# Kernel tuning notes

Measured on AMD Instinct MI355X. Metric: run time of the kernel, lower is better.

## Reference

```python
import jax, jax.numpy as jnp
import numpy as np

H = 512       # hidden_size
T_OUT = 168   # output_len


def _cell(x, h, c, Wih, Whh, b):
    # PyTorch LSTM cell, gate order (i, f, g, o); b = b_ih + b_hh merged.
    g = x @ Wih.T + h @ Whh.T + b
    i, f, gg, o = jnp.split(g, 4, axis=-1)
    c = jax.nn.sigmoid(f) * c + jax.nn.sigmoid(i) * jnp.tanh(gg)
    h = jax.nn.sigmoid(o) * jnp.tanh(c)
    return h, c


def setup_inputs() -> dict:
    key = jax.random.key(0)
    ks = jax.random.split(key, 20)
    B, T_IN, F = 1024, 336, 16
    s = 1.0 / np.sqrt(H)

    def w(k, shape):
        return (jax.random.normal(k, shape, dtype=jnp.float32) * s).astype(jnp.float32)

    return {
        "x": jax.random.normal(ks[0], (B, T_IN, F), dtype=jnp.float32),
        "enc_Wih0": w(ks[1], (4 * H, F)),
        "enc_Whh0": w(ks[2], (4 * H, H)),
        "enc_b0": w(ks[3], (4 * H,)),
        "enc_Wih1": w(ks[4], (4 * H, H)),
        "enc_Whh1": w(ks[5], (4 * H, H)),
        "enc_b1": w(ks[6], (4 * H,)),
        "dec_Wih0": w(ks[7], (4 * H, 1)),
        "dec_Whh0": w(ks[8], (4 * H, H)),
        "dec_b0": w(ks[9], (4 * H,)),
        "dec_Wih1": w(ks[10], (4 * H, H)),
        "dec_Whh1": w(ks[11], (4 * H, H)),
        "dec_b1": w(ks[12], (4 * H,)),
        "fc_W1": w(ks[13], (H // 2, H)),
        "fc_b1": w(ks[14], (H // 2,)),
        "fc_W2": w(ks[15], (1, H // 2)),
        "fc_b2": w(ks[16], (1,)),
    }


def reference(x, enc_Wih0, enc_Whh0, enc_b0, enc_Wih1, enc_Whh1, enc_b1,
              dec_Wih0, dec_Whh0, dec_b0, dec_Wih1, dec_Whh1, dec_b1,
              fc_W1, fc_b1, fc_W2, fc_b2):
    # Inference mode: no teacher forcing, dropout disabled (identity).
    B = x.shape[0]
    xs = jnp.swapaxes(x, 0, 1)  # [T_in, B, F]
    z = jnp.zeros((B, H), x.dtype)

    def enc_layer(seq, Wih, Whh, b):
        def step(carry, xt):
            h, c = carry
            h, c = _cell(xt, h, c, Wih, Whh, b)
            return (h, c), h
        (h, c), ys = jax.lax.scan(step, (z, z), seq)
        return ys, h, c

    ys0, h0, c0 = enc_layer(xs, enc_Wih0, enc_Whh0, enc_b0)
    _, h1, c1 = enc_layer(ys0, enc_Wih1, enc_Whh1, enc_b1)

    y0 = jnp.zeros((B, 1), x.dtype)  # decoder_input = zeros(batch,1,1) squeezed

    def dec_step(carry, _):
        h0, c0, h1, c1, y = carry
        h0, c0 = _cell(y, h0, c0, dec_Wih0, dec_Whh0, dec_b0)
        h1, c1 = _cell(h0, h1, c1, dec_Wih1, dec_Whh1, dec_b1)
        hid = jnp.maximum(h1 @ fc_W1.T + fc_b1, 0.0)
        pred = jnp.maximum(hid @ fc_W2.T + fc_b2, 0.0)  # [B, 1]
        return (h0, c0, h1, c1, pred), pred[:, 0]

    _, outs = jax.lax.scan(dec_step, (h0, c0, h1, c1, y0), None, length=T_OUT)
    return jnp.swapaxes(outs, 0, 1)  # [B, T_OUT]
```

## Files before the change

kernel.cpp:

```cpp
#include <hip/hip_runtime.h>
#include <math.h>

#define TPB 512
#define NBLK 256

typedef unsigned short u16;
typedef unsigned char u8;
typedef float f32x4 __attribute__((ext_vector_type(4)));
typedef short s16x8 __attribute__((ext_vector_type(8)));
typedef unsigned int u32x4 __attribute__((ext_vector_type(4)));
typedef unsigned int u32x2 __attribute__((ext_vector_type(2)));

__device__ __forceinline__ u16 f2bf(float f) {
  unsigned u = __float_as_uint(f);
  unsigned r = (u + 0x7FFFu + ((u >> 16) & 1u)) >> 16;
  return (u16)r;
}
__device__ __forceinline__ float bf2f(u16 b) { return __uint_as_float(((unsigned)b) << 16); }
__device__ __forceinline__ float sigm(float x) { return 1.f / (1.f + expf(-x)); }

__device__ __forceinline__ f32x4 mfma_bf16(s16x8 a, s16x8 b, f32x4 c) {
  return __builtin_amdgcn_mfma_f32_16x16x32_bf16(a, b, c, 0, 0, 0);
}

__device__ __forceinline__ unsigned pk2(unsigned wd, int j) {
  int b0 = ((int)(wd << ((3 - j) * 8))) >> 24;
  int b1 = ((int)(wd << ((2 - j) * 8))) >> 24;
  float f0 = (float)b0 * 0.0078125f;
  float f1 = (float)b1 * 0.0078125f;
  return (__float_as_uint(f0) >> 16) | (__float_as_uint(f1) & 0xFFFF0000u);
}
__device__ __forceinline__ s16x8 unpk8(u32x2 wv) {
  s16x8 o;
#pragma unroll
  for (int j = 0; j < 4; ++j) {
    int b0 = ((int)(wv[0] << ((3 - j) * 8))) >> 24;
    float f0 = (float)b0 * 0.0078125f;
    o[j] = (short)(__float_as_uint(f0) >> 16);
    int b1 = ((int)(wv[1] << ((3 - j) * 8))) >> 24;
    float f1 = (float)b1 * 0.0078125f;
    o[4 + j] = (short)(__float_as_uint(f1) >> 16);
  }
  return o;
}

__device__ __forceinline__ u32x4 ld_sc1_x4(const void* p) {
  u32x4 d;
  asm volatile("global_load_dwordx4 %0, %1, off sc1"
               : "=v"(d) : "v"((unsigned long long)p) : "memory");
  return d;
}
__device__ __forceinline__ u32x2 ld_sc1_x2(const void* p) {
  u32x2 d;
  asm volatile("global_load_dwordx2 %0, %1, off sc1"
               : "=v"(d) : "v"((unsigned long long)p) : "memory");
  return d;
}
__device__ __forceinline__ s16x8 ld_b16x8(const void* p) {
  s16x8 d;
  asm volatile("global_load_dwordx4 %0, %1, off"
               : "=v"(d) : "v"((unsigned long long)p) : "memory");
  return d;
}
__device__ __forceinline__ void st_sc1_x4(void* p, u32x4 v) {
  asm volatile("global_store_dwordx4 %0, %1, off sc1"
               :: "v"((unsigned long long)p), "v"(v) : "memory");
}
__device__ __forceinline__ void wait_vm0() { asm volatile("s_waitcnt vmcnt(0)" ::: "memory"); }
#define WAITVM(n) asm volatile("s_waitcnt vmcnt(" #n ")" ::: "memory")
__device__ __forceinline__ void pin(u32x4& v) { asm volatile("" : "+v"(v)); }
__device__ __forceinline__ void pin(u32x2& v) { asm volatile("" : "+v"(v)); }
__device__ __forceinline__ void pin(s16x8& v) { asm volatile("" : "+v"(v)); }

struct KParams {
  const float* x;
  float* out;
  unsigned long long* cx;
  unsigned long long* cg;
  u8* h0h[2]; u8* h1h[2];
  const u16 *we0h, *we0l;
  const u16 *we1h, *we1l;
  const u16 *wd0h, *wd0l;
  const u16 *wd1h, *wd1l;
  const u16 *wfh;
  const float *be0, *be1, *bd0, *bd1, *wyp;
  const float *fcb1, *fcw2, *fcb2;
};

__global__ void zero_ws(uint4* p, long n) {
  uint4 z = {0u, 0u, 0u, 0u};
  for (long i = (long)blockIdx.x * blockDim.x + threadIdx.x; i < n; i += (long)gridDim.x * blockDim.x)
    p[i] = z;
}

__global__ void prep_w(const float* __restrict__ Wih, const float* __restrict__ Whh,
                       const float* __restrict__ bias,
                       u16* __restrict__ dhi, u16* __restrict__ dlo,
                       float* __restrict__ bias_p, float* __restrict__ wy_p,
                       int mode, int nchunks) {
  long total = (long)nchunks * 2048 * 32;
  for (long i = (long)blockIdx.x * blockDim.x + threadIdx.x; i < total; i += (long)gridDim.x * blockDim.x) {
    int kk = (int)(i & 31);
    long r1 = i >> 5;
    int n = (int)(r1 & 2047);
    int c = (int)(r1 >> 11);
    int h = n >> 2, g = n & 3;
    int no = g * 512 + h;
    float wv;
    if (mode == 0)      wv = (c < 16) ? Whh[no * 512 + c * 32 + kk] : (kk < 16 ? Wih[no * 16 + kk] : 0.f);
    else if (mode == 1) wv = (c < 16) ? Wih[no * 512 + c * 32 + kk] : Whh[no * 512 + (c - 16) * 32 + kk];
    else                wv = Whh[no * 512 + c * 32 + kk];
    u16 hb = f2bf(wv);
    dhi[i] = hb;
    dlo[i] = f2bf(wv - bf2f(hb));
    if (i < 2048) {
      int nn = (int)i, hh = nn >> 2, gg = nn & 3, noo = gg * 512 + hh;
      bias_p[nn] = bias[noo];
      if (mode == 2) wy_p[nn] = Wih[noo];
    }
  }
}

__global__ void prep_fc(const float* __restrict__ W1, u16* __restrict__ dhi) {
  int total = 16 * 256 * 32;
  for (int i = blockIdx.x * blockDim.x + threadIdx.x; i < total; i += gridDim.x * blockDim.x) {
    int kk = i & 31, n = (i >> 5) & 255, c = i >> 13;
    dhi[i] = f2bf(W1[n * 512 + c * 32 + kk]);
  }
}

__device__ __forceinline__ void gbar(const KParams& P, int mgrp, unsigned long long bi) {
  wait_vm0();
  __syncthreads();
  if (threadIdx.x == 0) {
    unsigned long long* ctr = &P.cx[mgrp * 32];
    __hip_atomic_fetch_add(ctr, 1ULL, __ATOMIC_RELAXED, __HIP_MEMORY_SCOPE_AGENT);
    unsigned long long t0 = __builtin_amdgcn_s_memrealtime();
    while (__hip_atomic_load(ctr, __ATOMIC_RELAXED, __HIP_MEMORY_SCOPE_AGENT) < bi * 16ULL) {
      __builtin_amdgcn_s_sleep(2);
      if (__builtin_amdgcn_s_memrealtime() - t0 > 300000000ULL) {
        P.out[0] = 1e9f;
        break;
      }
    }
  }
  __syncthreads();
}

template <int NCT, bool TWOA, bool HASX, bool HASY>
__device__ __forceinline__ void lstm_phase(
    const KParams& P, int m_tile, int n_tile,
    const u8* A1h, const u8* A2h,
    const u16* WBh, const u16* WBl,
    const float* __restrict__ bias_p, const float* __restrict__ wyp, int t,
    float (&creg)[4], u8* Hh, char* smem, const float* yb) {
  constexpr int NST = NCT / 2;
  const int tid = threadIdx.x;
  const int w = tid >> 6, lane = tid & 63, r = lane & 15, q = lane >> 4;
  const int m0 = m_tile * 64, n0 = n_tile * 128;
  u16* sA = (u16*)smem;
  const int rr = (tid >> 2) & 63, seg = tid & 3, chA = tid >> 8;

  f32x4 acc[4];
#pragma unroll
  for (int mr = 0; mr < 4; ++mr) acc[mr] = (f32x4){0.f, 0.f, 0.f, 0.f};

  u32x2 ab[6];
  s16x8 bb[2][4];
  const int a_elem = (m0 + rr) * 32 + seg * 8;
  const int b_elem = (n0 + w * 16 + r) * 32 + q * 8;

  auto issueA = [&](int s) {
    int c = s * 2 + chA;
    const u8* base = A1h;
    if (TWOA && c >= 16) { base = A2h; c -= 16; }
    ab[s % 6] = ld_sc1_x2(base + c * 32768 + a_elem);
  };
  auto issueB = [&](int s) {
#pragma unroll
    for (int i = 0; i < 4; ++i) {
      int ch = i >> 1, hl = i & 1;
      int c = s * 2 + ch;
      bb[s & 1][i] = ld_b16x8((hl ? WBl : WBh) + c * 65536 + b_elem);
    }
  };

  issueA(0); issueB(0); issueA(1); issueB(1);
  issueA(2); issueA(3); issueA(4); issueA(5);

#pragma unroll
  for (int s = 0; s < NST; ++s) {
    if (s == NST - 1)       WAITVM(0);
    else if (s <= 1)        WAITVM(9);
    else if (s <= NST - 6)  WAITVM(6);
    else if (s == NST - 5)  WAITVM(5);
    else                    WAITVM(4);
    pin(ab[s % 6]);
#pragma unroll
    for (int i = 0; i < 4; ++i) pin(bb[s & 1][i]);
    u16* sAb = sA + (s & 1) * 5120;
    {
      u32x2 av = ab[s % 6];
      u32x4 w0;
      w0[0] = pk2(av[0], 0); w0[1] = pk2(av[0], 2);
      w0[2] = pk2(av[1], 0); w0[3] = pk2(av[1], 2);
      *(u32x4*)(sAb + (chA * 64 + rr) * 40 + seg * 8) = w0;
    }
    __syncthreads();
#pragma unroll
    for (int ch = 0; ch < 2; ++ch)
#pragma unroll
      for (int mr = 0; mr < 4; ++mr) {
        const s16x8 ah = *(const s16x8*)(sAb + (ch * 64 + mr * 16 + r) * 40 + q * 8);
        acc[mr] = mfma_bf16(ah, bb[s & 1][ch * 2 + 0], acc[mr]);
        acc[mr] = mfma_bf16(ah, bb[s & 1][ch * 2 + 1], acc[mr]);
      }
    if (s + 2 < NST) issueB(s + 2);
    if (s + 6 < NST) issueA(s + 6);
  }

  if (HASX) {
#pragma unroll
    for (int mr = 0; mr < 4; ++mr) {
      s16x8 axh;
#pragma unroll
      for (int j = 0; j < 8; ++j) axh[j] = 0;
      if (q < 2) {
        const float* xp = P.x + (((long)(m0 + mr * 16 + r) * 336 + t) * 16 + q * 8);
        float4 v0 = *(const float4*)xp;
        float4 v1 = *(const float4*)(xp + 4);
        float vv[8] = {v0.x, v0.y, v0.z, v0.w, v1.x, v1.y, v1.z, v1.w};
#pragma unroll
        for (int j = 0; j < 8; ++j) axh[j] = (short)f2bf(vv[j]);
      }
      long bo = ((long)16 * 2048 + n0 + w * 16 + r) * 32 + q * 8;
      acc[mr] = mfma_bf16(axh, *(const s16x8*)(WBh + bo), acc[mr]);
      acc[mr] = mfma_bf16(axh, *(const s16x8*)(WBl + bo), acc[mr]);
    }
  }

  __syncthreads();
  float* gbuf = (float*)smem;
#pragma unroll
  for (int mr = 0; mr < 4; ++mr)
#pragma unroll
    for (int reg = 0; reg < 4; ++reg)
      gbuf[(mr * 16 + q * 4 + reg) * 132 + (w * 16 + r)] = acc[mr][reg];
  __syncthreads();
  u8 hbv[4];
#pragma unroll
  for (int kk2 = 0; kk2 < 4; ++kk2) {
    int p = tid + kk2 * 512;
    int ml = p >> 5, hl2 = p & 31;
    f32x4 g4 = *(const f32x4*)(gbuf + ml * 132 + hl2 * 4);
    int nb = n0 + hl2 * 4;
    float g0 = g4[0] + bias_p[nb + 0];
    float g1 = g4[1] + bias_p[nb + 1];
    float g2 = g4[2] + bias_p[nb + 2];
    float g3 = g4[3] + bias_p[nb + 3];
    if (HASY) {
      float yv = yb[ml];
      g0 += yv * wyp[nb + 0];
      g1 += yv * wyp[nb + 1];
      g2 += yv * wyp[nb + 2];
      g3 += yv * wyp[nb + 3];
    }
    float ig = sigm(g0), fg = sigm(g1), gg = tanhf(g2), og = sigm(g3);
    float cn = fg * creg[kk2] + ig * gg;
    creg[kk2] = cn;
    int qi = __float2int_rn(og * tanhf(cn) * 128.f);
    qi = qi > 127 ? 127 : (qi < -127 ? -127 : qi);
    hbv[kk2] = (u8)qi;
  }
  __syncthreads();
  u8* lh = (u8*)smem;
#pragma unroll
  for (int kk2 = 0; kk2 < 4; ++kk2) {
    int p = tid + kk2 * 512;
    lh[(p >> 5) * 48 + (p & 31)] = hbv[kk2];
  }
  __syncthreads();
  if (tid < 128) {
    int rw = tid >> 1, sg = tid & 1;
    st_sc1_x4(Hh + (n_tile * 1024 + m0 + rw) * 32 + sg * 16,
              *(const u32x4*)(lh + rw * 48 + sg * 16));
  }
}

__device__ __forceinline__ void fc_inline(const KParams& P, int m_tile, int n_tile,
                                          const u8* Ah, int tOut, char* smem) {
  const int tid = threadIdx.x;
  const int w = tid >> 6, lane = tid & 63, r = lane & 15, q = lane >> 4;
  const int m0 = m_tile * 64;
  u8* sF = (u8*)smem;
  f32x4 af[4][2];
#pragma unroll
  for (int mr = 0; mr < 4; ++mr)
#pragma unroll
    for (int mi = 0; mi < 2; ++mi) af[mr][mi] = (f32x4){0.f, 0.f, 0.f, 0.f};

  u32x4 v1[2], v2[2];
#pragma unroll
  for (int j = 0; j < 2; ++j) {
    int idx = tid + j * 512;
    int c = idx >> 7, rw = (idx >> 1) & 63, sg = idx & 1;
    v1[j] = ld_sc1_x4(Ah + c * 32768 + (m0 + rw) * 32 + sg * 16);
  }
#pragma unroll
  for (int j = 0; j < 2; ++j) {
    int idx = tid + j * 512;
    int c = (idx >> 7) + 8, rw = (idx >> 1) & 63, sg = idx & 1;
    v2[j] = ld_sc1_x4(Ah + c * 32768 + (m0 + rw) * 32 + sg * 16);
  }
  WAITVM(2);
#pragma unroll
  for (int j = 0; j < 2; ++j) pin(v1[j]);
#pragma unroll
  for (int j = 0; j < 2; ++j) {
    int idx = tid + j * 512;
    int c = idx >> 7, rw = (idx >> 1) & 63, sg = idx & 1;
    *(u32x4*)(sF + (c * 64 + rw) * 48 + sg * 16) = v1[j];
  }
  __syncthreads();
#pragma unroll
  for (int pass = 0; pass < 2; ++pass) {
    for (int c = 0; c < 8; ++c)
#pragma unroll
      for (int mr = 0; mr < 4; ++mr) {
        const s16x8 ah = unpk8(*(const u32x2*)(sF + (c * 64 + mr * 16 + r) * 48 + q * 8));
#pragma unroll
        for (int mi = 0; mi < 2; ++mi) {
          int col = w * 32 + mi * 16 + r;
          af[mr][mi] = mfma_bf16(
              ah, *(const s16x8*)(P.wfh + ((pass * 8 + c) * 256 + col) * 32 + q * 8),
              af[mr][mi]);
        }
      }
    if (pass == 0) {
      wait_vm0();
#pragma unroll
      for (int j = 0; j < 2; ++j) pin(v2[j]);
      __syncthreads();
#pragma unroll
      for (int j = 0; j < 2; ++j) {
        int idx = tid + j * 512;
        int c = idx >> 7, rw = (idx >> 1) & 63, sg = idx & 1;
        *(u32x4*)(sF + (c * 64 + rw) * 48 + sg * 16) = v2[j];
      }
      __syncthreads();
    }
  }
  __syncthreads();
  u16* hidb = (u16*)smem;
#pragma unroll
  for (int mr = 0; mr < 4; ++mr)
#pragma unroll
    for (int mi = 0; mi < 2; ++mi)
#pragma unroll
      for (int reg = 0; reg < 4; ++reg) {
        int row = mr * 16 + q * 4 + reg, col = w * 32 + mi * 16 + r;
        hidb[row * 264 + col] = f2bf(fmaxf(af[mr][mi][reg] + P.fcb1[col], 0.f));
      }
  __syncthreads();
  float* part = (float*)(smem + 33792);
  if (tid < 256) {
    int m = tid >> 2, sg = tid & 3;
    float s = 0.f;
#pragma unroll
    for (int j = 0; j < 64; ++j)
      s += bf2f(hidb[m * 264 + sg * 64 + j]) * P.fcw2[sg * 64 + j];
    part[m * 5 + sg] = s;
  }
  __syncthreads();
  float* yb = (float*)(smem + 40960);
  if (tid < 64) {
    float s = P.fcb2[0] + part[tid * 5 + 0] + part[tid * 5 + 1] +
              part[tid * 5 + 2] + part[tid * 5 + 3];
    float pred = fmaxf(s, 0.f);
    yb[tid] = pred;
    if (n_tile == 0) P.out[(long)(m0 + tid) * 168 + tOut] = pred;
  }
  __syncthreads();
}

__global__ void __launch_bounds__(TPB, 2) lstm_seq(KParams P) {
  __shared__ __align__(16) char smem[41216];
  const int b = blockIdx.x;
  const int grp = b & 7;
  const int idx = b >> 3;
  const int n_tile = grp * 2 + (idx & 1);
  const int m_tile = idx >> 1;
  const float* yb = (const float*)(smem + 40960);
  unsigned long long bi = 0;
  int p0 = 0, p1 = 0;
  float c0r[4], c1r[4];
#pragma unroll
  for (int i = 0; i < 4; ++i) { c0r[i] = 0.f; c1r[i] = 0.f; }

  for (int p = 0; p <= 336; ++p) {
    if (p < 336)
      lstm_phase<16, false, true, false>(P, m_tile, n_tile, P.h0h[p0], nullptr,
                                         P.we0h, P.we0l, P.be0, nullptr, p, c0r,
                                         P.h0h[p0 ^ 1], smem, nullptr);
    if (p >= 1)
      lstm_phase<32, true, false, false>(P, m_tile, n_tile, P.h0h[p0], P.h1h[p1],
                                         P.we1h, P.we1l, P.be1, nullptr, 0, c1r,
                                         P.h1h[p1 ^ 1], smem, nullptr);
    if (p < 336) p0 ^= 1;
    if (p >= 1) p1 ^= 1;
    ++bi; gbar(P, m_tile, bi);
  }
  for (int t = 0; t < 168; ++t) {
    if (t > 0) {
      fc_inline(P, m_tile, n_tile, P.h1h[p1], t - 1, smem);
    } else {
      if (threadIdx.x < 64) ((float*)(smem + 40960))[threadIdx.x] = 0.f;
      __syncthreads();
    }
    lstm_phase<16, false, false, true>(P, m_tile, n_tile, P.h0h[p0], nullptr,
                                       P.wd0h, P.wd0l, P.bd0, P.wyp, 0, c0r,
                                       P.h0h[p0 ^ 1], smem, yb);
    p0 ^= 1; ++bi; gbar(P, m_tile, bi);
    lstm_phase<32, true, false, false>(P, m_tile, n_tile, P.h0h[p0], P.h1h[p1],
                                       P.wd1h, P.wd1l, P.bd1, nullptr, 0, c1r,
                                       P.h1h[p1 ^ 1], smem, nullptr);
    p1 ^= 1; ++bi; gbar(P, m_tile, bi);
  }
  fc_inline(P, m_tile, n_tile, P.h1h[p1], 167, smem);
}

extern "C" void kernel_launch(void* const* d_in, const int* in_sizes, int n_in,
                              void* d_out, int out_size, void* d_ws, size_t ws_size,
                              hipStream_t stream) {
  const float* x     = (const float*)d_in[0];
  const float* eWih0 = (const float*)d_in[1];
  const float* eWhh0 = (const float*)d_in[2];
  const float* eb0   = (const float*)d_in[3];
  const float* eWih1 = (const float*)d_in[4];
  const float* eWhh1 = (const float*)d_in[5];
  const float* eb1   = (const float*)d_in[6];
  const float* dWih0 = (const float*)d_in[7];
  const float* dWhh0 = (const float*)d_in[8];
  const float* db0   = (const float*)d_in[9];
  const float* dWih1 = (const float*)d_in[10];
  const float* dWhh1 = (const float*)d_in[11];
  const float* db1   = (const float*)d_in[12];
  const float* fcW1  = (const float*)d_in[13];
  const float* fcb1  = (const float*)d_in[14];
  const float* fcW2  = (const float*)d_in[15];
  const float* fcb2  = (const float*)d_in[16];

  char* ws = (char*)d_ws;
  unsigned long long* cx = (unsigned long long*)(ws + 0);
  unsigned long long* cg = (unsigned long long*)(ws + 4096);
  char* hb = ws + 8192;
  u8* h0h0 = (u8*)(hb + 0L * 1048576);
  u8* h0h1 = (u8*)(hb + 1L * 1048576);
  u8* h1h0 = (u8*)(hb + 2L * 1048576);
  u8* h1h1 = (u8*)(hb + 3L * 1048576);
  char* wb = hb + 4L * 1048576;
  u16* we0h = (u16*)wb; wb += 2228224L;
  u16* we0l = (u16*)wb; wb += 2228224L;
  u16* we1h = (u16*)wb; wb += 4194304L;
  u16* we1l = (u16*)wb; wb += 4194304L;
  u16* wd0h = (u16*)wb; wb += 2097152L;
  u16* wd0l = (u16*)wb; wb += 2097152L;
  u16* wd1h = (u16*)wb; wb += 4194304L;
  u16* wd1l = (u16*)wb; wb += 4194304L;
  u16* wfh  = (u16*)wb; wb += 262144L;
  float* be0 = (float*)wb; wb += 8192L;
  float* be1 = (float*)wb; wb += 8192L;
  float* bd0 = (float*)wb; wb += 8192L;
  float* bd1 = (float*)wb; wb += 8192L;
  float* wyp = (float*)wb; wb += 8192L;

  long zbytes = 8192L + 4L * 1048576L;
  zero_ws<<<1024, 256, 0, stream>>>((uint4*)ws, zbytes / 16);
  prep_w<<<2048, 256, 0, stream>>>(eWih0, eWhh0, eb0, we0h, we0l, be0, nullptr, 0, 17);
  prep_w<<<2048, 256, 0, stream>>>(eWih1, eWhh1, eb1, we1h, we1l, be1, nullptr, 1, 32);
  prep_w<<<2048, 256, 0, stream>>>(dWih0, dWhh0, db0, wd0h, wd0l, bd0, wyp, 2, 16);
  prep_w<<<2048, 256, 0, stream>>>(dWih1, dWhh1, db1, wd1h, wd1l, bd1, nullptr, 1, 32);
  prep_fc<<<512, 256, 0, stream>>>(fcW1, wfh);

  KParams P;
  P.x = x; P.out = (float*)d_out; P.cx = cx; P.cg = cg;
  P.h0h[0] = h0h0; P.h0h[1] = h0h1;
  P.h1h[0] = h1h0; P.h1h[1] = h1h1;
  P.we0h = we0h; P.we0l = we0l; P.we1h = we1h; P.we1l = we1l;
  P.wd0h = wd0h; P.wd0l = wd0l; P.wd1h = wd1h; P.wd1l = wd1l;
  P.wfh = wfh;
  P.be0 = be0; P.be1 = be1; P.bd0 = bd0; P.bd1 = bd1; P.wyp = wyp;
  P.fcb1 = fcb1; P.fcw2 = fcW2; P.fcb2 = fcb2;

  lstm_seq<<<NBLK, TPB, 0, stream>>>(P);
}
```

Measured before the change: 20.05 ms.

## Double threads per block to 1024 and split per-wave MFMA work across M

Raises the block size from 512 to 1024 threads. The 16 waves are arranged as a 2x8 grid over the 64x128 gate tile, so each wave handles 2 M-row tiles instead of 4. The FC stage likewise gives each wave one 16-column slice, and A loads shrink to one dword per thread. The aim is more latency hiding and shorter per-wave serial MFMA chains in this latency-bound persistent recurrent kernel. In exchange it adds register pressure under launch_bounds(1024,4), each B tile is now loaded by two waves, and __syncthreads barriers span more waves.

```diff
diff --git a/kernel.cpp b/kernel.cpp
--- a/kernel.cpp
+++ b/kernel.cpp
@@ -1,7 +1,7 @@
 #include <hip/hip_runtime.h>
 #include <math.h>
 
-#define TPB 512
+#define TPB 1024
 #define NBLK 256
 
 typedef unsigned short u16;
@@ -50,9 +50,9 @@
                : "=v"(d) : "v"((unsigned long long)p) : "memory");
   return d;
 }
-__device__ __forceinline__ u32x2 ld_sc1_x2(const void* p) {
-  u32x2 d;
-  asm volatile("global_load_dwordx2 %0, %1, off sc1"
+__device__ __forceinline__ unsigned ld_sc1_x1(const void* p) {
+  unsigned d;
+  asm volatile("global_load_dword %0, %1, off sc1"
                : "=v"(d) : "v"((unsigned long long)p) : "memory");
   return d;
 }
@@ -69,7 +69,7 @@
 __device__ __forceinline__ void wait_vm0() { asm volatile("s_waitcnt vmcnt(0)" ::: "memory"); }
 #define WAITVM(n) asm volatile("s_waitcnt vmcnt(" #n ")" ::: "memory")
 __device__ __forceinline__ void pin(u32x4& v) { asm volatile("" : "+v"(v)); }
-__device__ __forceinline__ void pin(u32x2& v) { asm volatile("" : "+v"(v)); }
+__device__ __forceinline__ void pin(unsigned& v) { asm volatile("" : "+v"(v)); }
 __device__ __forceinline__ void pin(s16x8& v) { asm volatile("" : "+v"(v)); }
 
 struct KParams {
@@ -153,28 +153,29 @@
     const u8* A1h, const u8* A2h,
     const u16* WBh, const u16* WBl,
     const float* __restrict__ bias_p, const float* __restrict__ wyp, int t,
-    float (&creg)[4], u8* Hh, char* smem, const float* yb) {
+    float (&creg)[2], u8* Hh, char* smem, const float* yb) {
   constexpr int NST = NCT / 2;
   const int tid = threadIdx.x;
   const int w = tid >> 6, lane = tid & 63, r = lane & 15, q = lane >> 4;
+  const int w_m = w >> 3, w_n = w & 7;
   const int m0 = m_tile * 64, n0 = n_tile * 128;
   u16* sA = (u16*)smem;
-  const int rr = (tid >> 2) & 63, seg = tid & 3, chA = tid >> 8;
-
-  f32x4 acc[4];
-#pragma unroll
-  for (int mr = 0; mr < 4; ++mr) acc[mr] = (f32x4){0.f, 0.f, 0.f, 0.f};
-
-  u32x2 ab[6];
+  const int rr = (tid >> 3) & 63, seg = tid & 7, chA = tid >> 9;
+
+  f32x4 acc[2];
+#pragma unroll
+  for (int mr = 0; mr < 2; ++mr) acc[mr] = (f32x4){0.f, 0.f, 0.f, 0.f};
+
+  unsigned ab[6];
   s16x8 bb[2][4];
-  const int a_elem = (m0 + rr) * 32 + seg * 8;
-  const int b_elem = (n0 + w * 16 + r) * 32 + q * 8;
+  const int a_elem = (m0 + rr) * 32 + seg * 4;
+  const int b_elem = (n0 + w_n * 16 + r) * 32 + q * 8;
 
   auto issueA = [&](int s) {
     int c = s * 2 + chA;
     const u8* base = A1h;
     if (TWOA && c >= 16) { base = A2h; c -= 16; }
-    ab[s % 6] = ld_sc1_x2(base + c * 32768 + a_elem);
+    ab[s % 6] = ld_sc1_x1(base + c * 32768 + a_elem);
   };
   auto issueB = [&](int s) {
 #pragma unroll
@@ -200,18 +201,18 @@
     for (int i = 0; i < 4; ++i) pin(bb[s & 1][i]);
     u16* sAb = sA + (s & 1) * 5120;
     {
-      u32x2 av = ab[s % 6];
-      u32x4 w0;
-      w0[0] = pk2(av[0], 0); w0[1] = pk2(av[0], 2);
-      w0[2] = pk2(av[1], 0); w0[3] = pk2(av[1], 2);
-      *(u32x4*)(sAb + (chA * 64 + rr) * 40 + seg * 8) = w0;
+      unsigned av = ab[s % 6];
+      u32x2 w0;
+      w0[0] = pk2(av, 0); w0[1] = pk2(av, 2);
+      *(u32x2*)(sAb + (chA * 64 + rr) * 40 + seg * 4) = w0;
     }
     __syncthreads();
 #pragma unroll
     for (int ch = 0; ch < 2; ++ch)
 #pragma unroll
-      for (int mr = 0; mr < 4; ++mr) {
-        const s16x8 ah = *(const s16x8*)(sAb + (ch * 64 + mr * 16 + r) * 40 + q * 8);
+      for (int mr = 0; mr < 2; ++mr) {
+        const s16x8 ah =
+            *(const s16x8*)(sAb + (ch * 64 + w_m * 32 + mr * 16 + r) * 40 + q * 8);
         acc[mr] = mfma_bf16(ah, bb[s & 1][ch * 2 + 0], acc[mr]);
         acc[mr] = mfma_bf16(ah, bb[s & 1][ch * 2 + 1], acc[mr]);
       }
@@ -221,19 +222,20 @@
 
   if (HASX) {
 #pragma unroll
-    for (int mr = 0; mr < 4; ++mr) {
+    for (int mr = 0; mr < 2; ++mr) {
       s16x8 axh;
 #pragma unroll
       for (int j = 0; j < 8; ++j) axh[j] = 0;
       if (q < 2) {
-        const float* xp = P.x + (((long)(m0 + mr * 16 + r) * 336 + t) * 16 + q * 8);
+        const float* xp =
+            P.x + (((long)(m0 + w_m * 32 + mr * 16 + r) * 336 + t) * 16 + q * 8);
         float4 v0 = *(const float4*)xp;
         float4 v1 = *(const float4*)(xp + 4);
         float vv[8] = {v0.x, v0.y, v0.z, v0.w, v1.x, v1.y, v1.z, v1.w};
 #pragma unroll
         for (int j = 0; j < 8; ++j) axh[j] = (short)f2bf(vv[j]);
       }
-      long bo = ((long)16 * 2048 + n0 + w * 16 + r) * 32 + q * 8;
+      long bo = ((long)16 * 2048 + n0 + w_n * 16 + r) * 32 + q * 8;
       acc[mr] = mfma_bf16(axh, *(const s16x8*)(WBh + bo), acc[mr]);
       acc[mr] = mfma_bf16(axh, *(const s16x8*)(WBl + bo), acc[mr]);
     }
@@ -242,15 +244,15 @@
   __syncthreads();
   float* gbuf = (float*)smem;
 #pragma unroll
-  for (int mr = 0; mr < 4; ++mr)
+  for (int mr = 0; mr < 2; ++mr)
 #pragma unroll
     for (int reg = 0; reg < 4; ++reg)
-      gbuf[(mr * 16 + q * 4 + reg) * 132 + (w * 16 + r)] = acc[mr][reg];
-  __syncthreads();
-  u8 hbv[4];
-#pragma unroll
-  for (int kk2 = 0; kk2 < 4; ++kk2) {
-    int p = tid + kk2 * 512;
+      gbuf[(w_m * 32 + mr * 16 + q * 4 + reg) * 132 + (w_n * 16 + r)] = acc[mr][reg];
+  __syncthreads();
+  u8 hbv[2];
+#pragma unroll
+  for (int kk2 = 0; kk2 < 2; ++kk2) {
+    int p = tid + kk2 * 1024;
     int ml = p >> 5, hl2 = p & 31;
     f32x4 g4 = *(const f32x4*)(gbuf + ml * 132 + hl2 * 4);
     int nb = n0 + hl2 * 4;
@@ -275,8 +277,8 @@
   __syncthreads();
   u8* lh = (u8*)smem;
 #pragma unroll
-  for (int kk2 = 0; kk2 < 4; ++kk2) {
-    int p = tid + kk2 * 512;
+  for (int kk2 = 0; kk2 < 2; ++kk2) {
+    int p = tid + kk2 * 1024;
     lh[(p >> 5) * 48 + (p & 31)] = hbv[kk2];
   }
   __syncthreads();
@@ -293,33 +295,21 @@
   const int w = tid >> 6, lane = tid & 63, r = lane & 15, q = lane >> 4;
   const int m0 = m_tile * 64;
   u8* sF = (u8*)smem;
-  f32x4 af[4][2];
-#pragma unroll
-  for (int mr = 0; mr < 4; ++mr)
-#pragma unroll
-    for (int mi = 0; mi < 2; ++mi) af[mr][mi] = (f32x4){0.f, 0.f, 0.f, 0.f};
-
-  u32x4 v1[2], v2[2];
-#pragma unroll
-  for (int j = 0; j < 2; ++j) {
-    int idx = tid + j * 512;
-    int c = idx >> 7, rw = (idx >> 1) & 63, sg = idx & 1;
-    v1[j] = ld_sc1_x4(Ah + c * 32768 + (m0 + rw) * 32 + sg * 16);
-  }
-#pragma unroll
-  for (int j = 0; j < 2; ++j) {
-    int idx = tid + j * 512;
-    int c = (idx >> 7) + 8, rw = (idx >> 1) & 63, sg = idx & 1;
-    v2[j] = ld_sc1_x4(Ah + c * 32768 + (m0 + rw) * 32 + sg * 16);
-  }
-  WAITVM(2);
-#pragma unroll
-  for (int j = 0; j < 2; ++j) pin(v1[j]);
-#pragma unroll
-  for (int j = 0; j < 2; ++j) {
-    int idx = tid + j * 512;
-    int c = idx >> 7, rw = (idx >> 1) & 63, sg = idx & 1;
-    *(u32x4*)(sF + (c * 64 + rw) * 48 + sg * 16) = v1[j];
+  f32x4 af[4];
+#pragma unroll
+  for (int mr = 0; mr < 4; ++mr) af[mr] = (f32x4){0.f, 0.f, 0.f, 0.f};
+
+  u32x4 v1, v2;
+  {
+    int c = tid >> 7, rw = (tid >> 1) & 63, sg = tid & 1;
+    v1 = ld_sc1_x4(Ah + c * 32768 + (m0 + rw) * 32 + sg * 16);
+    v2 = ld_sc1_x4(Ah + (c + 8) * 32768 + (m0 + rw) * 32 + sg * 16);
+  }
+  WAITVM(1);
+  pin(v1);
+  {
+    int c = tid >> 7, rw = (tid >> 1) & 63, sg = tid & 1;
+    *(u32x4*)(sF + (c * 64 + rw) * 48 + sg * 16) = v1;
   }
   __syncthreads();
 #pragma unroll
@@ -328,24 +318,18 @@
 #pragma unroll
       for (int mr = 0; mr < 4; ++mr) {
         const s16x8 ah = unpk8(*(const u32x2*)(sF + (c * 64 + mr * 16 + r) * 48 + q * 8));
-#pragma unroll
-        for (int mi = 0; mi < 2; ++mi) {
-          int col = w * 32 + mi * 16 + r;
-          af[mr][mi] = mfma_bf16(
-              ah, *(const s16x8*)(P.wfh + ((pass * 8 + c) * 256 + col) * 32 + q * 8),
-              af[mr][mi]);
-        }
+        int col = w * 16 + r;
+        af[mr] = mfma_bf16(
+            ah, *(const s16x8*)(P.wfh + ((pass * 8 + c) * 256 + col) * 32 + q * 8),
+            af[mr]);
       }
     if (pass == 0) {
       wait_vm0();
-#pragma unroll
-      for (int j = 0; j < 2; ++j) pin(v2[j]);
+      pin(v2);
       __syncthreads();
-#pragma unroll
-      for (int j = 0; j < 2; ++j) {
-        int idx = tid + j * 512;
-        int c = idx >> 7, rw = (idx >> 1) & 63, sg = idx & 1;
-        *(u32x4*)(sF + (c * 64 + rw) * 48 + sg * 16) = v2[j];
+      {
+        int c = tid >> 7, rw = (tid >> 1) & 63, sg = tid & 1;
+        *(u32x4*)(sF + (c * 64 + rw) * 48 + sg * 16) = v2;
       }
       __syncthreads();
     }
@@ -355,12 +339,10 @@
 #pragma unroll
   for (int mr = 0; mr < 4; ++mr)
 #pragma unroll
-    for (int mi = 0; mi < 2; ++mi)
-#pragma unroll
-      for (int reg = 0; reg < 4; ++reg) {
-        int row = mr * 16 + q * 4 + reg, col = w * 32 + mi * 16 + r;
-        hidb[row * 264 + col] = f2bf(fmaxf(af[mr][mi][reg] + P.fcb1[col], 0.f));
-      }
+    for (int reg = 0; reg < 4; ++reg) {
+      int row = mr * 16 + q * 4 + reg, col = w * 16 + r;
+      hidb[row * 264 + col] = f2bf(fmaxf(af[mr][reg] + P.fcb1[col], 0.f));
+    }
   __syncthreads();
   float* part = (float*)(smem + 33792);
   if (tid < 256) {
@@ -383,7 +365,7 @@
   __syncthreads();
 }
 
-__global__ void __launch_bounds__(TPB, 2) lstm_seq(KParams P) {
+__global__ void __launch_bounds__(TPB, 4) lstm_seq(KParams P) {
   __shared__ __align__(16) char smem[41216];
   const int b = blockIdx.x;
   const int grp = b & 7;
@@ -393,9 +375,9 @@
   const float* yb = (const float*)(smem + 40960);
   unsigned long long bi = 0;
   int p0 = 0, p1 = 0;
-  float c0r[4], c1r[4];
-#pragma unroll
-  for (int i = 0; i < 4; ++i) { c0r[i] = 0.f; c1r[i] = 0.f; }
+  float c0r[2], c1r[2];
+#pragma unroll
+  for (int i = 0; i < 2; ++i) { c0r[i] = 0.f; c1r[i] = 0.f; }
 
   for (int p = 0; p <= 336; ++p) {
     if (p < 336)
```

After: 30.35 ms. 1.51x slower.
